# Kernel optimization log

Hardware: AMD Instinct MI355X
Metric: run time of the kernel (lower is better)

## Reference

```python
import jax, jax.numpy as jnp
import numpy as np

D = 1024      # model dimension
H = 16        # heads
DK = D // H   # head dim
DFF = 4096    # ffn hidden
B, S = 2, 2048
EPS = 1e-6
NEG_SLOPE = 0.01  # torch LeakyReLU default


def setup_inputs() -> dict:
    key = jax.random.key(0)
    ks = jax.random.split(key, 12)
    sd = 1.0 / np.sqrt(D)
    sf = 1.0 / np.sqrt(DFF)
    return {
        "x": jax.random.normal(ks[0], (B, S, D), dtype=jnp.float32),
        "wq": jax.random.uniform(ks[1], (D, D), jnp.float32, -sd, sd),
        "bq": jnp.zeros((D,), jnp.float32),
        "wk": jax.random.uniform(ks[2], (D, D), jnp.float32, -sd, sd),
        "bk": jnp.zeros((D,), jnp.float32),
        "wv": jax.random.uniform(ks[3], (D, D), jnp.float32, -sd, sd),
        "bv": jnp.zeros((D,), jnp.float32),
        "wo": jax.random.uniform(ks[4], (D, D), jnp.float32, -sd, sd),
        "bo": jnp.zeros((D,), jnp.float32),
        "g1": jnp.ones((D,), jnp.float32),
        "b1": jnp.zeros((D,), jnp.float32),
        "w_ff1": jax.random.uniform(ks[5], (D, DFF), jnp.float32, -sd, sd),
        "b_ff1": jnp.zeros((DFF,), jnp.float32),
        "w_ff2": jax.random.uniform(ks[6], (DFF, D), jnp.float32, -sf, sf),
        "b_ff2": jnp.zeros((D,), jnp.float32),
        "g2": jnp.ones((D,), jnp.float32),
        "b2": jnp.zeros((D,), jnp.float32),
    }


def _layernorm(x, g, b):
    mu = jnp.mean(x, axis=-1, keepdims=True)
    var = jnp.mean(jnp.square(x - mu), axis=-1, keepdims=True)
    return (x - mu) * jax.lax.rsqrt(var + EPS) * g + b


def reference(x, wq, bq, wk, bk, wv, bv, wo, bo, g1, b1,
              w_ff1, b_ff1, w_ff2, b_ff2, g2, b2):
    # Multi-head attention
    q = (x @ wq + bq).reshape(B, S, H, DK).transpose(0, 2, 1, 3)  # [B,H,S,DK]
    k = (x @ wk + bk).reshape(B, S, H, DK).transpose(0, 2, 1, 3)
    v = (x @ wv + bv).reshape(B, S, H, DK).transpose(0, 2, 1, 3)
    scores = jnp.einsum('bhqd,bhkd->bhqk', q, k) / np.sqrt(DK)
    attn = jax.nn.softmax(scores, axis=-1)
    ctx = jnp.einsum('bhqk,bhkd->bhqd', attn, v)
    ctx = ctx.transpose(0, 2, 1, 3).reshape(B, S, D)
    attn_out = ctx @ wo + bo
    # residual + LN1 (dropout = identity in eval)
    h = _layernorm(attn_out + x, g1, b1)
    # FFN with LeakyReLU
    ff = jnp.where(h @ w_ff1 + b_ff1 > 0,
                   h @ w_ff1 + b_ff1,
                   NEG_SLOPE * (h @ w_ff1 + b_ff1))
    ff = ff @ w_ff2 + b_ff2
    return _layernorm(ff + h, g2, b2)
```

## Files before the change

### kernel.cpp

```cpp
#include <hip/hip_runtime.h>
#include <math.h>

#define D_MODEL 1024
#define NHEAD   16
#define DKH     64
#define DFF_    4096
#define BB      2
#define SS      2048
#define MTOT    (BB*SS)
#define EPSLN   1e-6f
#define NEG_SLOPE 0.01f

typedef unsigned short u16;
typedef unsigned int   u32;
typedef __bf16 bf16x8 __attribute__((ext_vector_type(8)));
typedef float  f32x4  __attribute__((ext_vector_type(4)));
typedef u16    u16x4  __attribute__((ext_vector_type(4)));

__device__ __forceinline__ u16 f2bf(float f) {
    u32 u = __float_as_uint(f);
    u = (u + 0x7fffu + ((u >> 16) & 1u)) >> 16;
    return (u16)u;
}
__device__ __forceinline__ float bf2f(u16 u) {
    return __uint_as_float(((u32)u) << 16);
}

__device__ __forceinline__ void gload_lds16(const u16* g, u16* l) {
    __builtin_amdgcn_global_load_lds(
        (const __attribute__((address_space(1))) u32*)g,
        (__attribute__((address_space(3))) u32*)l,
        16, 0, 0);
}

__device__ __forceinline__ void transpose_tile(const float* __restrict__ W,
        u16* __restrict__ WT, int N, int out_stride, int out_row_off,
        float scale, int bx, int by, u16* T)
{
    const int t  = threadIdx.x;
    const int n0 = bx * 64;
    const int k0 = by * 64;
    #pragma unroll
    for (int i = 0; i < 4; ++i) {
        int r = i * 16 + (t >> 4);
        int c = (t & 15) * 4;
        float4 v = *(const float4*)&W[(size_t)(k0 + r) * N + n0 + c];
        T[(c + 0) * 72 + r] = f2bf(v.x * scale);
        T[(c + 1) * 72 + r] = f2bf(v.y * scale);
        T[(c + 2) * 72 + r] = f2bf(v.z * scale);
        T[(c + 3) * 72 + r] = f2bf(v.w * scale);
    }
    __syncthreads();
    #pragma unroll
    for (int i = 0; i < 4; ++i) {
        int nr = i * 16 + (t >> 4);
        int kc = (t & 15) * 4;
        u16x4 o = { T[nr*72 + kc], T[nr*72 + kc + 1], T[nr*72 + kc + 2], T[nr*72 + kc + 3] };
        *(u16x4*)&WT[(size_t)(out_row_off + n0 + nr) * out_stride + k0 + kc] = o;
    }
}

__global__ __launch_bounds__(256)
void prep(const float* __restrict__ x, u16* __restrict__ x_bf,
          const float* __restrict__ wq, const float* __restrict__ wk,
          const float* __restrict__ wv, const float* __restrict__ wo,
          const float* __restrict__ wff1, const float* __restrict__ wff2,
          u16* __restrict__ wqkvT, u16* __restrict__ woT,
          u16* __restrict__ wff1T, u16* __restrict__ wff2T,
          const float* __restrict__ bq, const float* __restrict__ bk,
          const float* __restrict__ bv, float* __restrict__ qkv_bias,
          float qscale)
{
    __shared__ u16 T[64 * 72];
    int blk = blockIdx.x;
    if (blk < 4096) {
        int i = blk * 256 + threadIdx.x;
        float4 v = ((const float4*)x)[i];
        u16x4 o = { f2bf(v.x), f2bf(v.y), f2bf(v.z), f2bf(v.w) };
        ((u16x4*)x_bf)[i] = o;
        return;
    }
    blk -= 4096;
    if (blk < 1024) {
        int which = blk >> 8, r = blk & 255;
        const float* Ws = which == 0 ? wq : which == 1 ? wk : which == 2 ? wv : wo;
        u16* Wd   = which == 3 ? woT : wqkvT;
        int off   = which == 3 ? 0 : which * 1024;
        float sc  = which == 0 ? qscale : 1.0f;
        transpose_tile(Ws, Wd, 1024, 1024, off, sc, r & 15, r >> 4, T);
        return;
    }
    blk -= 1024;
    if (blk < 1024) {
        transpose_tile(wff1, wff1T, 4096, 1024, 0, 1.0f, blk & 63, blk >> 6, T);
        return;
    }
    blk -= 1024;
    if (blk < 1024) {
        transpose_tile(wff2, wff2T, 1024, 4096, 0, 1.0f, blk & 15, blk >> 4, T);
        return;
    }
    blk -= 1024;
    int i = blk * 256 + threadIdx.x;
    qkv_bias[i] = (i < 1024) ? bq[i] * qscale
                : (i < 2048) ? bk[i - 1024] : bv[i - 2048];
}

template<int EPI>
__global__ __launch_bounds__(256)
void gemm_bf16(const u16* __restrict__ A, const u16* __restrict__ BT,
               const float* __restrict__ bias, void* __restrict__ Cout,
               u16* __restrict__ Vt, int M, int N, int k_len, int kstride)
{
    __shared__ u16 As[128 * 32];
    __shared__ u16 Bs[128 * 32];
    const int tid  = threadIdx.x;
    const int w    = tid >> 6;
    const int lane = tid & 63;
    const int lm   = lane & 15;
    const int lq   = lane >> 4;
    const int row0 = blockIdx.y * 128;
    const int col0 = blockIdx.x * 128;
    const int k_off = blockIdx.z * k_len;
    const int wrow = (w >> 1) * 64;
    const int wcol = (w & 1) * 64;

    f32x4 acc[4][4] = {};

    const int r_l  = lane >> 2;
    const int q_sw = (lane & 3) ^ ((lane >> 3) & 3);
    const u16* a_src = A  + (size_t)(row0 + w * 32 + r_l) * kstride + k_off + q_sw * 8;
    const u16* b_src = BT + (size_t)(col0 + w * 32 + r_l) * kstride + k_off + q_sw * 8;
    u16* a_dst = &As[(w * 32) * 32];
    u16* b_dst = &Bs[(w * 32) * 32];
    const size_t stepA = (size_t)16 * kstride;

    const int pos = lq ^ ((lm >> 1) & 3);
    const u16* a_rd = &As[(wrow + lm) * 32 + pos * 8];
    const u16* b_rd = &Bs[(wcol + lm) * 32 + pos * 8];

    for (int k0 = 0; k0 < k_len; k0 += 32) {
        gload_lds16(a_src + k0,         a_dst);
        gload_lds16(a_src + k0 + stepA, a_dst + 16 * 32);
        gload_lds16(b_src + k0,         b_dst);
        gload_lds16(b_src + k0 + stepA, b_dst + 16 * 32);
        __syncthreads();
        bf16x8 av[4], bv[4];
        #pragma unroll
        for (int m = 0; m < 4; ++m) av[m] = *(const bf16x8*)(a_rd + m * 16 * 32);
        #pragma unroll
        for (int n = 0; n < 4; ++n) bv[n] = *(const bf16x8*)(b_rd + n * 16 * 32);
        #pragma unroll
        for (int m = 0; m < 4; ++m)
            #pragma unroll
            for (int n = 0; n < 4; ++n)
                acc[m][n] = __builtin_amdgcn_mfma_f32_16x16x32_bf16(av[m], bv[n], acc[m][n], 0, 0, 0);
        __syncthreads();
    }

    float bz[4] = {0.f, 0.f, 0.f, 0.f};
    if (EPI != 3) {
        #pragma unroll
        for (int n = 0; n < 4; ++n) bz[n] = bias[col0 + wcol + n * 16 + lm];
    }

    if (EPI == 4 && col0 >= 2048) {
        #pragma unroll
        for (int m = 0; m < 4; ++m) {
            int rbase = row0 + wrow + m * 16 + lq * 4;
            int b = rbase >> 11, s = rbase & 2047;
            #pragma unroll
            for (int n = 0; n < 4; ++n) {
                int c = col0 + wcol + n * 16 + lm - 2048;
                u16x4 pk = { f2bf(acc[m][n][0] + bz[n]), f2bf(acc[m][n][1] + bz[n]),
                             f2bf(acc[m][n][2] + bz[n]), f2bf(acc[m][n][3] + bz[n]) };
                *(u16x4*)&Vt[(size_t)((b * 16 + (c >> 6)) * 64 + (c & 63)) * 2048 + s] = pk;
            }
        }
        return;
    }

    u16* Cz = (u16*)Cout + (EPI == 3 ? (size_t)blockIdx.z * M * N : 0);
    #pragma unroll
    for (int m = 0; m < 4; ++m) {
        #pragma unroll
        for (int e = 0; e < 4; ++e) {
            int row = row0 + wrow + m * 16 + lq * 4 + e;
            #pragma unroll
            for (int n = 0; n < 4; ++n) {
                int col = col0 + wcol + n * 16 + lm;
                float v = acc[m][n][e] + bz[n];
                if (EPI == 1) v = v > 0.f ? v : NEG_SLOPE * v;
                Cz[(size_t)row * N + col] = f2bf(v);
            }
        }
    }
}

__global__ __launch_bounds__(256)
void attn_mfma(const u16* __restrict__ QKV, const u16* __restrict__ Vt,
               u16* __restrict__ ctx)
{
    __shared__ u16 Qs[64 * 72];
    __shared__ u16 Ks[64 * 72];
    __shared__ u16 Vs[64 * 72];
    __shared__ u16 Ps[64 * 72];
    const int tid = threadIdx.x, w = tid >> 6, lane = tid & 63;
    const int lm = lane & 15, lq = lane >> 4;
    const int q0 = blockIdx.x * 64;
    const int bh = blockIdx.y;
    const int b  = bh >> 4, h = bh & 15;
    const size_t row_b = (size_t)b * SS;
    const int ccol = h * DKH;

    const int sr = tid >> 3;
    const int sc = (tid & 7) * 8;

    #pragma unroll
    for (int i = 0; i < 2; ++i) {
        int r = i * 32 + sr;
        *(bf16x8*)&Qs[r * 72 + sc] =
            *(const bf16x8*)(QKV + (row_b + q0 + r) * 3072 + ccol + sc);
    }
    bf16x8 kr[2], vr[2];
    #pragma unroll
    for (int i = 0; i < 2; ++i) {
        int r = i * 32 + sr;
        kr[i] = *(const bf16x8*)(QKV + (row_b + r) * 3072 + 1024 + ccol + sc);
        vr[i] = *(const bf16x8*)(Vt + ((size_t)bh * 64 + r) * SS + sc);
    }
    __syncthreads();
    bf16x8 aq0 = *(const bf16x8*)&Qs[(w * 16 + lm) * 72 + lq * 8];
    bf16x8 aq1 = *(const bf16x8*)&Qs[(w * 16 + lm) * 72 + 32 + lq * 8];

    bf16x8 ones;
    #pragma unroll
    for (int j = 0; j < 8; ++j) ones[j] = (__bf16)1.0f;

    f32x4 o[4] = {};
    f32x4 lacc = {};

    for (int kt = 0; kt < SS / 64; ++kt) {
        __syncthreads();
        #pragma unroll
        for (int i = 0; i < 2; ++i) {
            int r = i * 32 + sr;
            *(bf16x8*)&Ks[r * 72 + sc] = kr[i];
            *(bf16x8*)&Vs[r * 72 + sc] = vr[i];
        }
        const int kn = ((kt + 1) & 31) * 64;
        #pragma unroll
        for (int i = 0; i < 2; ++i) {
            int r = i * 32 + sr;
            kr[i] = *(const bf16x8*)(QKV + (row_b + kn + r) * 3072 + 1024 + ccol + sc);
            vr[i] = *(const bf16x8*)(Vt + ((size_t)bh * 64 + r) * SS + kn + sc);
        }
        __syncthreads();

        f32x4 s[4] = {};
        #pragma unroll
        for (int n = 0; n < 4; ++n) {
            bf16x8 bk0 = *(const bf16x8*)&Ks[(n * 16 + lm) * 72 + lq * 8];
            bf16x8 bk1 = *(const bf16x8*)&Ks[(n * 16 + lm) * 72 + 32 + lq * 8];
            s[n] = __builtin_amdgcn_mfma_f32_16x16x32_bf16(aq0, bk0, s[n], 0, 0, 0);
            s[n] = __builtin_amdgcn_mfma_f32_16x16x32_bf16(aq1, bk1, s[n], 0, 0, 0);
        }
        const int prow = (w * 16 + lq * 4) * 72 + lm;
        #pragma unroll
        for (int n = 0; n < 4; ++n)
            #pragma unroll
            for (int e = 0; e < 4; ++e) {
                float p = __builtin_exp2f(s[n][e]);
                Ps[prow + e * 72 + n * 16] =
                    (u16)((__float_as_uint(p) + 0x8000u) >> 16);
            }
        __syncthreads();

        bf16x8 ap0 = *(const bf16x8*)&Ps[(w * 16 + lm) * 72 + lq * 8];
        bf16x8 ap1 = *(const bf16x8*)&Ps[(w * 16 + lm) * 72 + 32 + lq * 8];
        #pragma unroll
        for (int n = 0; n < 4; ++n) {
            bf16x8 bv0 = *(const bf16x8*)&Vs[(n * 16 + lm) * 72 + lq * 8];
            bf16x8 bv1 = *(const bf16x8*)&Vs[(n * 16 + lm) * 72 + 32 + lq * 8];
            o[n] = __builtin_amdgcn_mfma_f32_16x16x32_bf16(ap0, bv0, o[n], 0, 0, 0);
            o[n] = __builtin_amdgcn_mfma_f32_16x16x32_bf16(ap1, bv1, o[n], 0, 0, 0);
        }
        lacc = __builtin_amdgcn_mfma_f32_16x16x32_bf16(ap0, ones, lacc, 0, 0, 0);
        lacc = __builtin_amdgcn_mfma_f32_16x16x32_bf16(ap1, ones, lacc, 0, 0, 0);
    }

    #pragma unroll
    for (int e = 0; e < 4; ++e) {
        float inv = 1.0f / lacc[e];
        int row = q0 + w * 16 + lq * 4 + e;
        u16* dst = ctx + (row_b + row) * D_MODEL + ccol;
        #pragma unroll
        for (int n = 0; n < 4; ++n)
            dst[n * 16 + lm] = f2bf(o[n][e] * inv);
    }
}

template<int OUTF32, int RESBF>
__global__ __launch_bounds__(256)
void add_ln(const u16* __restrict__ C0, const u16* __restrict__ C1,
            const float* __restrict__ cbias, const void* __restrict__ resid,
            const float* __restrict__ g, const float* __restrict__ beta,
            float* __restrict__ outf, u16* __restrict__ outb)
{
    __shared__ float red[8];
    const int row = blockIdx.x;
    const int tid = threadIdx.x;
    u16x4 p0 = ((const u16x4*)(C0 + (size_t)row * D_MODEL))[tid];
    u16x4 p1 = ((const u16x4*)(C1 + (size_t)row * D_MODEL))[tid];
    float4 cb = ((const float4*)cbias)[tid];
    float4 rr;
    if (RESBF) {
        u16x4 rb = ((const u16x4*)((const u16*)resid + (size_t)row * D_MODEL))[tid];
        rr = { bf2f(rb.x), bf2f(rb.y), bf2f(rb.z), bf2f(rb.w) };
    } else {
        rr = ((const float4*)((const float*)resid + (size_t)row * D_MODEL))[tid];
    }
    float4 v = { bf2f(p0.x) + bf2f(p1.x) + cb.x + rr.x,
                 bf2f(p0.y) + bf2f(p1.y) + cb.y + rr.y,
                 bf2f(p0.z) + bf2f(p1.z) + cb.z + rr.z,
                 bf2f(p0.w) + bf2f(p1.w) + cb.w + rr.w };
    float s  = v.x + v.y + v.z + v.w;
    float sq = v.x*v.x + v.y*v.y + v.z*v.z + v.w*v.w;
    #pragma unroll
    for (int off = 32; off > 0; off >>= 1) {
        s  += __shfl_down(s,  off, 64);
        sq += __shfl_down(sq, off, 64);
    }
    const int wv = tid >> 6;
    if ((tid & 63) == 0) { red[wv] = s; red[4 + wv] = sq; }
    __syncthreads();
    float st  = red[0] + red[1] + red[2] + red[3];
    float sqt = red[4] + red[5] + red[6] + red[7];
    float mu   = st * (1.0f / D_MODEL);
    float var  = sqt * (1.0f / D_MODEL) - mu * mu;
    float rstd = rsqrtf(var + EPSLN);
    float4 gv = ((const float4*)g)[tid];
    float4 bt = ((const float4*)beta)[tid];
    float4 ov;
    ov.x = (v.x - mu) * rstd * gv.x + bt.x;
    ov.y = (v.y - mu) * rstd * gv.y + bt.y;
    ov.z = (v.z - mu) * rstd * gv.z + bt.z;
    ov.w = (v.w - mu) * rstd * gv.w + bt.w;
    if (OUTF32) {
        ((float4*)(outf + (size_t)row * D_MODEL))[tid] = ov;
    } else {
        u16x4 ob = { f2bf(ov.x), f2bf(ov.y), f2bf(ov.z), f2bf(ov.w) };
        ((u16x4*)(outb + (size_t)row * D_MODEL))[tid] = ob;
    }
}

extern "C" void kernel_launch(void* const* d_in, const int* in_sizes, int n_in,
                              void* d_out, int out_size, void* d_ws, size_t ws_size,
                              hipStream_t stream) {
    const float* x     = (const float*)d_in[0];
    const float* wq    = (const float*)d_in[1];
    const float* bq    = (const float*)d_in[2];
    const float* wk    = (const float*)d_in[3];
    const float* bk    = (const float*)d_in[4];
    const float* wv    = (const float*)d_in[5];
    const float* bv    = (const float*)d_in[6];
    const float* wo    = (const float*)d_in[7];
    const float* bo    = (const float*)d_in[8];
    const float* g1    = (const float*)d_in[9];
    const float* b1    = (const float*)d_in[10];
    const float* w_ff1 = (const float*)d_in[11];
    const float* b_ff1 = (const float*)d_in[12];
    const float* w_ff2 = (const float*)d_in[13];
    const float* b_ff2 = (const float*)d_in[14];
    const float* g2    = (const float*)d_in[15];
    const float* b2    = (const float*)d_in[16];
    float* out = (float*)d_out;

    const float qscale = 0.18033688011112042f;

    char* W = (char*)d_ws;
    u16*   x_bf    = (u16*)(W + 0);
    u16*   wqkvT   = (u16*)(W + 8388608);
    u16*   woT     = (u16*)(W + 14680064);
    u16*   wff1T   = (u16*)(W + 16777216);
    u16*   wff2T   = (u16*)(W + 25165824);
    u16*   QKV     = (u16*)(W + 33554432);
    u16*   VtG     = (u16*)(W + 58720256);
    u16*   C0      = (u16*)(W + 67108864);
    u16*   C1      = (u16*)(W + 75497472);
    u16*   h_bf    = (u16*)(W + 83886080);
    float* qkv_bias= (float*)(W + 92274688);
    u16*   ctx     = x_bf;
    u16*   ff1_bf  = QKV;

    dim3 blk(256);
    prep<<<7180, blk, 0, stream>>>(x, x_bf, wq, wk, wv, wo, w_ff1, w_ff2,
                                   wqkvT, woT, wff1T, wff2T,
                                   bq, bk, bv, qkv_bias, qscale);
    gemm_bf16<4><<<dim3(24, 32, 1), blk, 0, stream>>>(x_bf, wqkvT, qkv_bias, QKV, VtG, MTOT, 3072, 1024, 1024);
    attn_mfma<<<dim3(32, 32), blk, 0, stream>>>(QKV, VtG, ctx);
    gemm_bf16<3><<<dim3(8, 32, 2), blk, 0, stream>>>(ctx, woT, nullptr, C0, nullptr, MTOT, 1024, 512, 1024);
    add_ln<0, 0><<<MTOT, blk, 0, stream>>>(C0, C1, bo, x, g1, b1, nullptr, h_bf);
    gemm_bf16<1><<<dim3(32, 32, 1), blk, 0, stream>>>(h_bf, wff1T, b_ff1, ff1_bf, nullptr, MTOT, DFF_, 1024, 1024);
    gemm_bf16<3><<<dim3(8, 32, 2), blk, 0, stream>>>(ff1_bf, wff2T, nullptr, C0, nullptr, MTOT, 1024, 2048, 4096);
    add_ln<1, 1><<<MTOT, blk, 0, stream>>>(C0, C1, b_ff2, h_bf, g2, b2, out, nullptr);
}
```

Baseline: 386.5 us.

## Double K tile in GEMM and double-buffer attention K/V via direct LDS loads

The GEMM kernel now stages 64-wide K slices per iteration with an XOR-swizzled 64-column LDS layout, which halves the number of barriers per K. The attention kernel replaces register-staged K/V copies with direct global-to-LDS loads into double buffers, issuing the next tile's loads before computing on the current one. It also merges the Q and P buffers and drops two barriers per iteration. The cost is more LDS per block, and the P write/read within a wave now relies on no barrier between them.

```diff
diff --git a/kernel.cpp b/kernel.cpp
--- a/kernel.cpp
+++ b/kernel.cpp
@@ -112,8 +112,8 @@
                const float* __restrict__ bias, void* __restrict__ Cout,
                u16* __restrict__ Vt, int M, int N, int k_len, int kstride)
 {
-    __shared__ u16 As[128 * 32];
-    __shared__ u16 Bs[128 * 32];
+    __shared__ u16 As[128 * 64];
+    __shared__ u16 Bs[128 * 64];
     const int tid  = threadIdx.x;
     const int w    = tid >> 6;
     const int lane = tid & 63;
@@ -127,34 +127,39 @@
 
     f32x4 acc[4][4] = {};
 
-    const int r_l  = lane >> 2;
-    const int q_sw = (lane & 3) ^ ((lane >> 3) & 3);
-    const u16* a_src = A  + (size_t)(row0 + w * 32 + r_l) * kstride + k_off + q_sw * 8;
-    const u16* b_src = BT + (size_t)(col0 + w * 32 + r_l) * kstride + k_off + q_sw * 8;
-    u16* a_dst = &As[(w * 32) * 32];
-    u16* b_dst = &Bs[(w * 32) * 32];
-    const size_t stepA = (size_t)16 * kstride;
-
-    const int pos = lq ^ ((lm >> 1) & 3);
-    const u16* a_rd = &As[(wrow + lm) * 32 + pos * 8];
-    const u16* b_rd = &Bs[(wcol + lm) * 32 + pos * 8];
-
-    for (int k0 = 0; k0 < k_len; k0 += 32) {
-        gload_lds16(a_src + k0,         a_dst);
-        gload_lds16(a_src + k0 + stepA, a_dst + 16 * 32);
-        gload_lds16(b_src + k0,         b_dst);
-        gload_lds16(b_src + k0 + stepA, b_dst + 16 * 32);
+    const int r_i = lane >> 3;
+    const int csw = ((lane & 7) ^ r_i) * 8;
+    const u16* a_src = A  + (size_t)(row0 + w * 32 + r_i) * kstride + k_off + csw;
+    const u16* b_src = BT + (size_t)(col0 + w * 32 + r_i) * kstride + k_off + csw;
+    u16* a_dst = &As[(w * 32) * 64];
+    u16* b_dst = &Bs[(w * 32) * 64];
+
+    const int fr0 = (lq ^ (lm & 7)) * 8;
+    const int fr1 = ((4 + lq) ^ (lm & 7)) * 8;
+    const u16* a_rd = &As[(wrow + lm) * 64];
+    const u16* b_rd = &Bs[(wcol + lm) * 64];
+
+    for (int k0 = 0; k0 < k_len; k0 += 64) {
+        #pragma unroll
+        for (int i = 0; i < 4; ++i) {
+            gload_lds16(a_src + k0 + (size_t)(i * 8) * kstride, a_dst + (i * 8) * 64);
+            gload_lds16(b_src + k0 + (size_t)(i * 8) * kstride, b_dst + (i * 8) * 64);
+        }
         __syncthreads();
-        bf16x8 av[4], bv[4];
-        #pragma unroll
-        for (int m = 0; m < 4; ++m) av[m] = *(const bf16x8*)(a_rd + m * 16 * 32);
-        #pragma unroll
-        for (int n = 0; n < 4; ++n) bv[n] = *(const bf16x8*)(b_rd + n * 16 * 32);
-        #pragma unroll
-        for (int m = 0; m < 4; ++m)
-            #pragma unroll
-            for (int n = 0; n < 4; ++n)
-                acc[m][n] = __builtin_amdgcn_mfma_f32_16x16x32_bf16(av[m], bv[n], acc[m][n], 0, 0, 0);
+        #pragma unroll
+        for (int h = 0; h < 2; ++h) {
+            const int fo = h ? fr1 : fr0;
+            bf16x8 av[4], bv[4];
+            #pragma unroll
+            for (int m = 0; m < 4; ++m) av[m] = *(const bf16x8*)(a_rd + m * 16 * 64 + fo);
+            #pragma unroll
+            for (int n = 0; n < 4; ++n) bv[n] = *(const bf16x8*)(b_rd + n * 16 * 64 + fo);
+            #pragma unroll
+            for (int m = 0; m < 4; ++m)
+                #pragma unroll
+                for (int n = 0; n < 4; ++n)
+                    acc[m][n] = __builtin_amdgcn_mfma_f32_16x16x32_bf16(av[m], bv[n], acc[m][n], 0, 0, 0);
+        }
         __syncthreads();
     }
 
@@ -201,10 +206,9 @@
 void attn_mfma(const u16* __restrict__ QKV, const u16* __restrict__ Vt,
                u16* __restrict__ ctx)
 {
-    __shared__ u16 Qs[64 * 72];
-    __shared__ u16 Ks[64 * 72];
-    __shared__ u16 Vs[64 * 72];
-    __shared__ u16 Ps[64 * 72];
+    __shared__ u16 QP[64 * 72];
+    __shared__ u16 Kb[2][64 * 64];
+    __shared__ u16 Vb[2][64 * 64];
     const int tid = threadIdx.x, w = tid >> 6, lane = tid & 63;
     const int lm = lane & 15, lq = lane >> 4;
     const int q0 = blockIdx.x * 64;
@@ -213,25 +217,26 @@
     const size_t row_b = (size_t)b * SS;
     const int ccol = h * DKH;
 
-    const int sr = tid >> 3;
-    const int sc = (tid & 7) * 8;
-
+    const int r_i = lane >> 3;
+    const int csw = ((lane & 7) ^ r_i) * 8;
+    const u16* ksrc = QKV + (row_b + w * 16 + r_i) * 3072 + 1024 + ccol + csw;
+    const u16* vsrc = Vt + ((size_t)bh * 64 + w * 16 + r_i) * SS + csw;
+    const u16* qsrc = QKV + (row_b + q0 + w * 16 + r_i) * 3072 + ccol + csw;
+
+    gload_lds16(qsrc,                    &QP[(w * 16) * 64]);
+    gload_lds16(qsrc + (size_t)8 * 3072, &QP[(w * 16 + 8) * 64]);
     #pragma unroll
     for (int i = 0; i < 2; ++i) {
-        int r = i * 32 + sr;
-        *(bf16x8*)&Qs[r * 72 + sc] =
-            *(const bf16x8*)(QKV + (row_b + q0 + r) * 3072 + ccol + sc);
-    }
-    bf16x8 kr[2], vr[2];
-    #pragma unroll
-    for (int i = 0; i < 2; ++i) {
-        int r = i * 32 + sr;
-        kr[i] = *(const bf16x8*)(QKV + (row_b + r) * 3072 + 1024 + ccol + sc);
-        vr[i] = *(const bf16x8*)(Vt + ((size_t)bh * 64 + r) * SS + sc);
+        gload_lds16(ksrc + (size_t)(i * 8) * 3072, &Kb[0][(w * 16 + i * 8) * 64]);
+        gload_lds16(vsrc + (size_t)(i * 8) * SS,   &Vb[0][(w * 16 + i * 8) * 64]);
     }
     __syncthreads();
-    bf16x8 aq0 = *(const bf16x8*)&Qs[(w * 16 + lm) * 72 + lq * 8];
-    bf16x8 aq1 = *(const bf16x8*)&Qs[(w * 16 + lm) * 72 + 32 + lq * 8];
+
+    const int fr0 = (lq ^ (lm & 7)) * 8;
+    const int fr1 = ((4 + lq) ^ (lm & 7)) * 8;
+    bf16x8 aq0 = *(const bf16x8*)&QP[(w * 16 + lm) * 64 + fr0];
+    bf16x8 aq1 = *(const bf16x8*)&QP[(w * 16 + lm) * 64 + fr1];
+    __syncthreads();
 
     bf16x8 ones;
     #pragma unroll
@@ -241,27 +246,21 @@
     f32x4 lacc = {};
 
     for (int kt = 0; kt < SS / 64; ++kt) {
-        __syncthreads();
-        #pragma unroll
-        for (int i = 0; i < 2; ++i) {
-            int r = i * 32 + sr;
-            *(bf16x8*)&Ks[r * 72 + sc] = kr[i];
-            *(bf16x8*)&Vs[r * 72 + sc] = vr[i];
-        }
-        const int kn = ((kt + 1) & 31) * 64;
-        #pragma unroll
-        for (int i = 0; i < 2; ++i) {
-            int r = i * 32 + sr;
-            kr[i] = *(const bf16x8*)(QKV + (row_b + kn + r) * 3072 + 1024 + ccol + sc);
-            vr[i] = *(const bf16x8*)(Vt + ((size_t)bh * 64 + r) * SS + kn + sc);
-        }
-        __syncthreads();
-
+        const int cur = kt & 1;
+        if (kt < SS / 64 - 1) {
+            const int nxt = cur ^ 1;
+            const size_t koff = (size_t)(kt + 1) * 64;
+            #pragma unroll
+            for (int i = 0; i < 2; ++i) {
+                gload_lds16(ksrc + (koff + i * 8) * 3072, &Kb[nxt][(w * 16 + i * 8) * 64]);
+                gload_lds16(vsrc + koff + (size_t)(i * 8) * SS, &Vb[nxt][(w * 16 + i * 8) * 64]);
+            }
+        }
         f32x4 s[4] = {};
         #pragma unroll
         for (int n = 0; n < 4; ++n) {
-            bf16x8 bk0 = *(const bf16x8*)&Ks[(n * 16 + lm) * 72 + lq * 8];
-            bf16x8 bk1 = *(const bf16x8*)&Ks[(n * 16 + lm) * 72 + 32 + lq * 8];
+            bf16x8 bk0 = *(const bf16x8*)&Kb[cur][(n * 16 + lm) * 64 + fr0];
+            bf16x8 bk1 = *(const bf16x8*)&Kb[cur][(n * 16 + lm) * 64 + fr1];
             s[n] = __builtin_amdgcn_mfma_f32_16x16x32_bf16(aq0, bk0, s[n], 0, 0, 0);
             s[n] = __builtin_amdgcn_mfma_f32_16x16x32_bf16(aq1, bk1, s[n], 0, 0, 0);
         }
@@ -271,22 +270,21 @@
             #pragma unroll
             for (int e = 0; e < 4; ++e) {
                 float p = __builtin_exp2f(s[n][e]);
-                Ps[prow + e * 72 + n * 16] =
+                QP[prow + e * 72 + n * 16] =
                     (u16)((__float_as_uint(p) + 0x8000u) >> 16);
             }
-        __syncthreads();
-
-        bf16x8 ap0 = *(const bf16x8*)&Ps[(w * 16 + lm) * 72 + lq * 8];
-        bf16x8 ap1 = *(const bf16x8*)&Ps[(w * 16 + lm) * 72 + 32 + lq * 8];
+        bf16x8 ap0 = *(const bf16x8*)&QP[(w * 16 + lm) * 72 + lq * 8];
+        bf16x8 ap1 = *(const bf16x8*)&QP[(w * 16 + lm) * 72 + 32 + lq * 8];
         #pragma unroll
         for (int n = 0; n < 4; ++n) {
-            bf16x8 bv0 = *(const bf16x8*)&Vs[(n * 16 + lm) * 72 + lq * 8];
-            bf16x8 bv1 = *(const bf16x8*)&Vs[(n * 16 + lm) * 72 + 32 + lq * 8];
+            bf16x8 bv0 = *(const bf16x8*)&Vb[cur][(n * 16 + lm) * 64 + fr0];
+            bf16x8 bv1 = *(const bf16x8*)&Vb[cur][(n * 16 + lm) * 64 + fr1];
             o[n] = __builtin_amdgcn_mfma_f32_16x16x32_bf16(ap0, bv0, o[n], 0, 0, 0);
             o[n] = __builtin_amdgcn_mfma_f32_16x16x32_bf16(ap1, bv1, o[n], 0, 0, 0);
         }
         lacc = __builtin_amdgcn_mfma_f32_16x16x32_bf16(ap0, ones, lacc, 0, 0, 0);
         lacc = __builtin_amdgcn_mfma_f32_16x16x32_bf16(ap1, ones, lacc, 0, 0, 0);
+        __syncthreads();
     }
 
     #pragma unroll
```

New measurement: 382.1 us. About the same (-1.1%).
